# Kernel optimization log

Hardware: AMD Instinct MI355X
Metric: run time of the kernel (lower is better)

Reference implementation:

```python
import jax, jax.numpy as jnp
import numpy as np
from jax import lax

# Problem sizes (see shape_source)
B, N, S, K = 16, 4096, 1024, 32   # clouds, points/cloud, fps samples/cloud, max neighbors
C_IN, H1, H2, C_OUT = 64, 64, 64, 128
R = 0.2                            # radius ball query radius


def setup_inputs() -> dict:
    key = jax.random.key(0)
    ks = jax.random.split(key, 6)
    x = jax.random.normal(ks[0], (B * N, C_IN), jnp.float32)
    pos = jax.random.uniform(ks[1], (B * N, 3), jnp.float32)  # unit cube
    batch = jnp.repeat(jnp.arange(B, dtype=jnp.int32), N)     # equal-size clouds
    def lin(k, fan_in, fan_out):
        return jax.random.normal(k, (fan_in, fan_out), jnp.float32) / np.float32(np.sqrt(fan_in))
    W1 = lin(ks[2], C_IN + 3, H1); b1 = jnp.zeros((H1,), jnp.float32)
    W2 = lin(ks[3], H1, H2);      b2 = jnp.zeros((H2,), jnp.float32)
    W3 = lin(ks[4], H2, C_OUT);   b3 = jnp.zeros((C_OUT,), jnp.float32)
    return dict(x=x, pos=pos, batch=batch, W1=W1, b1=b1, W2=W2, b2=b2, W3=W3, b3=b3)


def _fps_single(pos):
    """Farthest point sampling on one cloud. pos: [N,3] -> [S] int32 indices.
    Deterministic start at index 0 (random_start=False equivalent)."""
    def step(carry, _):
        mind, last = carry
        d = jnp.sum((pos - pos[last]) ** 2, axis=-1)   # [N]
        mind = jnp.minimum(mind, d)
        nxt = jnp.argmax(mind).astype(jnp.int32)
        return (mind, nxt), last
    init = (jnp.full((pos.shape[0],), jnp.inf, pos.dtype), jnp.int32(0))
    _, idx = lax.scan(step, init, None, length=S)
    return idx  # [S]


def _radius_single(pos, qpos):
    """Ball query: for each query return up to K in-radius neighbors (first K by
    point index, matching torch_cluster's 'first found' semantics).
    pos: [N,3], qpos: [S,3] -> (nbr [S,K] int32, mask [S,K] bool)."""
    d2 = jnp.sum((qpos[:, None, :] - pos[None, :, :]) ** 2, axis=-1)   # [S,N]
    valid = d2 <= R * R
    key = jnp.where(valid, jnp.arange(N, dtype=jnp.int32), jnp.int32(N))  # invalid -> sentinel N
    neg_key, nbr = lax.top_k(-key, K)        # K smallest keys == first K valid indices
    mask = (-neg_key) < N
    nbr = jnp.where(mask, nbr, 0).astype(jnp.int32)  # safe gather index
    return nbr, mask


def reference(x, pos, batch, W1, b1, W2, b2, W3, b3):
    xb = x.reshape(B, N, C_IN)
    posb = pos.reshape(B, N, 3)

    # 1) FPS sampling per cloud
    idx = jax.vmap(_fps_single)(posb)                                   # [B,S]
    qpos = jnp.take_along_axis(posb, idx[:, :, None], axis=1)           # [B,S,3]

    # 2) radius ball query (max 32 neighbors)
    nbr, mask = jax.vmap(_radius_single)(posb, qpos)                    # [B,S,K]

    # 3) PointNetConv: gather, relative pos, MLP, masked max-scatter
    flat = nbr.reshape(B, S * K)
    xj = jnp.take_along_axis(xb, flat[:, :, None], axis=1).reshape(B, S, K, C_IN)
    pj = jnp.take_along_axis(posb, flat[:, :, None], axis=1).reshape(B, S, K, 3)
    rel = pj - qpos[:, :, None, :]                                      # pos_j - pos_i
    h = jnp.concatenate([xj, rel], axis=-1)                             # [B,S,K,C_IN+3]
    h = jax.nn.relu(h @ W1 + b1)
    h = jax.nn.relu(h @ W2 + b2)
    h = h @ W3 + b3                                                     # [B,S,K,C_OUT]
    h = jnp.where(mask[..., None], h, -jnp.inf)
    agg = jnp.max(h, axis=2)                                            # max aggregation
    agg = jnp.where(jnp.any(mask, axis=2)[..., None], agg, 0.0)         # empty -> 0
    out = jax.nn.relu(agg)                                              # [B,S,C_OUT]

    new_batch = jnp.repeat(jnp.arange(B, dtype=batch.dtype), S)
    return out.reshape(B * S, C_OUT), qpos.reshape(B * S, 3), new_batch
```

## Files before the change

kernel.cpp:

```cpp
#include <hip/hip_runtime.h>
#include <cstdint>
#include <cstddef>

#define B_    16
#define N_    4096
#define S_    1024
#define K_    32
#define COUT_ 128
#define NQ_   (B_*S_)

#define FT 256
#define FP (N_/FT)

__device__ __forceinline__ uint64_t wave_max_u64(uint64_t key) {
  uint32_t lo = (uint32_t)key, hi = (uint32_t)(key >> 32);
#define DPP_STEP(ctrl) { \
    uint32_t lo2 = (uint32_t)__builtin_amdgcn_update_dpp((int)lo, (int)lo, (ctrl), 0xf, 0xf, false); \
    uint32_t hi2 = (uint32_t)__builtin_amdgcn_update_dpp((int)hi, (int)hi, (ctrl), 0xf, 0xf, false); \
    const bool gt = (hi2 > hi) || (hi2 == hi && lo2 > lo); \
    hi = gt ? hi2 : hi; lo = gt ? lo2 : lo; \
  }
  DPP_STEP(0x111)
  DPP_STEP(0x112)
  DPP_STEP(0x114)
  DPP_STEP(0x118)
  DPP_STEP(0x142)
  DPP_STEP(0x143)
#undef DPP_STEP
  hi = (uint32_t)__builtin_amdgcn_readlane((int)hi, 63);
  lo = (uint32_t)__builtin_amdgcn_readlane((int)lo, 63);
  return ((uint64_t)hi << 32) | lo;
}

__global__ __launch_bounds__(FT) void fps_kernel(
    const float* __restrict__ pos, float* __restrict__ qpos_out,
    float* __restrict__ batch_out)
{
  __shared__ float px[N_], py[N_], pz[N_];
  __shared__ int   hist[S_];
  __shared__ uint64_t wkeys[2][FT/64];

  const int t = threadIdx.x;
  const int blk = blockIdx.x;
  const float* pb = pos + (size_t)blk * N_ * 3;

  for (int i = t; i < N_; i += FT) {
    px[i] = pb[i*3+0]; py[i] = pb[i*3+1]; pz[i] = pb[i*3+2];
  }
  for (int s = t; s < S_; s += FT) batch_out[(size_t)blk*S_ + s] = (float)blk;
  __syncthreads();

  float rx[FP], ry[FP], rz[FP], mind[FP];
  #pragma unroll
  for (int k = 0; k < FP; ++k) {
    const int p = k*FT + t;
    rx[k] = px[p]; ry[k] = py[p]; rz[k] = pz[p];
    mind[k] = INFINITY;
  }

  int last = 0;
  for (int s = 0; s < S_; ++s) {
    if (t == 0) hist[s] = last;
    if (s == S_-1) break;
    const float lx = px[last], ly = py[last], lz = pz[last];
    uint64_t best = 0;
    #pragma unroll
    for (int k = 0; k < FP; ++k) {
      #pragma clang fp contract(off)
      const float dx = rx[k]-lx;
      const float dy = ry[k]-ly;
      const float dz = rz[k]-lz;
      const float d  = dx*dx + dy*dy + dz*dz;
      const float m  = fminf(mind[k], d);
      mind[k] = m;
      const uint64_t key = ((uint64_t)__float_as_uint(m) << 32)
                         | (uint32_t)((N_-1) - (k*FT + t));
      if (key > best) best = key;
    }
    best = wave_max_u64(best);
    if ((t & 63) == 0) wkeys[s & 1][t >> 6] = best;
    __syncthreads();
    uint64_t gb = wkeys[s & 1][0];
    #pragma unroll
    for (int w = 1; w < FT/64; ++w) {
      const uint64_t o = wkeys[s & 1][w];
      if (o > gb) gb = o;
    }
    last = (N_-1) - (int)(uint32_t)gb;
  }
  __syncthreads();
  for (int s = t; s < S_; s += FT) {
    const int p = hist[s];
    qpos_out[((size_t)blk*S_ + s)*3 + 0] = px[p];
    qpos_out[((size_t)blk*S_ + s)*3 + 1] = py[p];
    qpos_out[((size_t)blk*S_ + s)*3 + 2] = pz[p];
  }
}

__global__ __launch_bounds__(256) void radius_kernel(
    const float* __restrict__ pos, const float* __restrict__ qpos,
    int* __restrict__ nbr, int* __restrict__ cnt_out)
{
  const int lane = threadIdx.x & 63;
  const int q = blockIdx.x * 4 + (threadIdx.x >> 6);
  const int b = q >> 10;
  const float* pb = pos + (size_t)b * N_ * 3;
  const float qx = qpos[(size_t)q*3+0];
  const float qy = qpos[(size_t)q*3+1];
  const float qz = qpos[(size_t)q*3+2];
  int cnt = 0;
  for (int base = 0; base < N_; base += 64) {
    #pragma clang fp contract(off)
    const int i = base + lane;
    const float dx = qx - pb[i*3+0];
    const float dy = qy - pb[i*3+1];
    const float dz = qz - pb[i*3+2];
    const float d  = dx*dx + dy*dy + dz*dz;
    const bool valid = (d <= 0.04f);
    const unsigned long long bal = __ballot(valid);
    const int below = __popcll(bal & ((1ull << lane) - 1ull));
    const int p = cnt + below;
    if (valid && p < K_) nbr[(size_t)q*K_ + p] = i;
    cnt += __popcll(bal);
    if (cnt >= K_) break;
  }
  const int c = (cnt < K_) ? cnt : K_;
  if (lane >= c && lane < K_) nbr[(size_t)q*K_ + lane] = 0;
  if (lane == 0) cnt_out[q] = c;
}

__global__ __launch_bounds__(256) void xw_kernel(
    const float* __restrict__ x, const float* __restrict__ W1,
    float* __restrict__ xw)
{
  __shared__ float xs[64*65];
  __shared__ float ws[64*64];
  const int t = threadIdx.x;
  const size_t rowbase = (size_t)blockIdx.x * 64;
  for (int k = t; k < 4096; k += 256) {
    xs[(k >> 6)*65 + (k & 63)] = x[rowbase*64 + k];
    ws[k] = W1[k];
  }
  __syncthreads();
  const int rg = t >> 4, cg = t & 15;
  const int r0 = rg*4, c0 = cg*4;
  float acc[4][4] = {};
  for (int i = 0; i < 64; ++i) {
    const float4 w = *(const float4*)&ws[i*64 + c0];
    #pragma unroll
    for (int j = 0; j < 4; ++j) {
      const float a = xs[(r0+j)*65 + i];
      acc[j][0] = fmaf(a, w.x, acc[j][0]);
      acc[j][1] = fmaf(a, w.y, acc[j][1]);
      acc[j][2] = fmaf(a, w.z, acc[j][2]);
      acc[j][3] = fmaf(a, w.w, acc[j][3]);
    }
  }
  #pragma unroll
  for (int j = 0; j < 4; ++j) {
    float4 v; v.x=acc[j][0]; v.y=acc[j][1]; v.z=acc[j][2]; v.w=acc[j][3];
    *(float4*)&xw[(rowbase + r0 + j)*64 + c0] = v;
  }
}

__global__ __launch_bounds__(256) void conv_kernel(
    const float* __restrict__ pos, const float* __restrict__ qpos,
    const int* __restrict__ nbr, const int* __restrict__ cnt,
    const float* __restrict__ xw,
    const float* __restrict__ W1, const float* __restrict__ b1,
    const float* __restrict__ W2, const float* __restrict__ b2,
    const float* __restrict__ W3, const float* __restrict__ b3,
    float* __restrict__ out)
{
  __shared__ float h1s[64*68];
  __shared__ float h2s[64*68];
  __shared__ float red[8*128];
  __shared__ int   nbrs[64];
  __shared__ float qps[8];
  __shared__ int   cnts[2];

  const int t  = threadIdx.x;
  const int q0 = blockIdx.x * 2;
  const int b  = q0 >> 10;

  if (t < 64) nbrs[t] = nbr[(size_t)q0*K_ + t];
  if (t < 2)  cnts[t] = cnt[q0 + t];
  if (t < 6)  qps[(t/3)*4 + (t%3)] = qpos[(size_t)q0*3 + t];
  __syncthreads();

  {
    const int c = t & 63;
    const int rsub = t >> 6;
    const float w1x = W1[64*64 + c];
    const float w1y = W1[65*64 + c];
    const float w1z = W1[66*64 + c];
    const float b1v = b1[c];
    #pragma unroll
    for (int it = 0; it < 16; ++it) {
      const int row = it*4 + rsub;
      const int lq  = row >> 5;
      const int j   = nbrs[row];
      const size_t gp = (size_t)b*N_ + j;
      const float xv = xw[gp*64 + c];
      const float rx = pos[gp*3+0] - qps[lq*4+0];
      const float ry = pos[gp*3+1] - qps[lq*4+1];
      const float rz = pos[gp*3+2] - qps[lq*4+2];
      float h = fmaf(rx, w1x, xv);
      h = fmaf(ry, w1y, h);
      h = fmaf(rz, w1z, h);
      h += b1v;
      h1s[row*68 + c] = fmaxf(h, 0.0f);
    }
  }
  __syncthreads();

  {
    const int rg = t >> 4, cg = t & 15;
    const int r0 = rg*4, c0 = cg*4;
    float acc[4][4] = {};
    for (int i = 0; i < 64; i += 4) {
      float a[4][4];
      #pragma unroll
      for (int j = 0; j < 4; ++j)
        *(float4*)&a[j][0] = *(const float4*)&h1s[(r0+j)*68 + i];
      #pragma unroll
      for (int di = 0; di < 4; ++di) {
        const float4 w = *(const float4*)&W2[(i+di)*64 + c0];
        #pragma unroll
        for (int j = 0; j < 4; ++j) {
          const float av = a[j][di];
          acc[j][0] = fmaf(av, w.x, acc[j][0]);
          acc[j][1] = fmaf(av, w.y, acc[j][1]);
          acc[j][2] = fmaf(av, w.z, acc[j][2]);
          acc[j][3] = fmaf(av, w.w, acc[j][3]);
        }
      }
    }
    const float4 bb = *(const float4*)&b2[c0];
    #pragma unroll
    for (int j = 0; j < 4; ++j) {
      float4 v;
      v.x = fmaxf(acc[j][0] + bb.x, 0.0f);
      v.y = fmaxf(acc[j][1] + bb.y, 0.0f);
      v.z = fmaxf(acc[j][2] + bb.z, 0.0f);
      v.w = fmaxf(acc[j][3] + bb.w, 0.0f);
      *(float4*)&h2s[(r0+j)*68 + c0] = v;
    }
  }
  __syncthreads();

  {
    const int rg = t >> 5, cg = t & 31;
    const int r0 = rg*8, c0 = cg*4;
    const int lq = rg >> 2;
    const int cq = cnts[lq];
    float acc[8][4] = {};
    for (int i = 0; i < 64; i += 4) {
      float a[8][4];
      #pragma unroll
      for (int j = 0; j < 8; ++j)
        *(float4*)&a[j][0] = *(const float4*)&h2s[(r0+j)*68 + i];
      #pragma unroll
      for (int di = 0; di < 4; ++di) {
        const float4 w = *(const float4*)&W3[(size_t)(i+di)*128 + c0];
        #pragma unroll
        for (int j = 0; j < 8; ++j) {
          const float av = a[j][di];
          acc[j][0] = fmaf(av, w.x, acc[j][0]);
          acc[j][1] = fmaf(av, w.y, acc[j][1]);
          acc[j][2] = fmaf(av, w.z, acc[j][2]);
          acc[j][3] = fmaf(av, w.w, acc[j][3]);
        }
      }
    }
    float pm0=-INFINITY, pm1=-INFINITY, pm2=-INFINITY, pm3=-INFINITY;
    #pragma unroll
    for (int j = 0; j < 8; ++j) {
      const int n = (r0 + j) & 31;
      if (n < cq) {
        pm0 = fmaxf(pm0, acc[j][0]);
        pm1 = fmaxf(pm1, acc[j][1]);
        pm2 = fmaxf(pm2, acc[j][2]);
        pm3 = fmaxf(pm3, acc[j][3]);
      }
    }
    float4 v; v.x=pm0; v.y=pm1; v.z=pm2; v.w=pm3;
    *(float4*)&red[rg*128 + c0] = v;
  }
  __syncthreads();
  {
    const int q = t >> 7, c = t & 127;
    const int cq = cnts[q];
    float v = -INFINITY;
    #pragma unroll
    for (int j = 0; j < 4; ++j) v = fmaxf(v, red[(q*4+j)*128 + c]);
    v = (cq > 0) ? (v + b3[c]) : 0.0f;
    v = fmaxf(v, 0.0f);
    out[(size_t)(q0 + q)*COUT_ + c] = v;
  }
}

extern "C" void kernel_launch(void* const* d_in, const int* in_sizes, int n_in,
                              void* d_out, int out_size, void* d_ws, size_t ws_size,
                              hipStream_t stream) {
  const float* x   = (const float*)d_in[0];
  const float* pos = (const float*)d_in[1];
  const float* W1  = (const float*)d_in[3];
  const float* b1  = (const float*)d_in[4];
  const float* W2  = (const float*)d_in[5];
  const float* b2  = (const float*)d_in[6];
  const float* W3  = (const float*)d_in[7];
  const float* b3  = (const float*)d_in[8];

  float* out    = (float*)d_out;
  float* qpos   = out + (size_t)NQ_*COUT_;
  float* batchf = qpos + (size_t)NQ_*3;

  char* ws = (char*)d_ws;
  float* xw = (float*)ws;
  int* nbr  = (int*)(ws + (size_t)B_*N_*64*sizeof(float));
  int* cnt  = nbr + (size_t)NQ_*K_;

  hipLaunchKernelGGL(xw_kernel,     dim3((B_*N_)/64), dim3(256), 0, stream, x, W1, xw);
  hipLaunchKernelGGL(fps_kernel,    dim3(B_),         dim3(FT),  0, stream, pos, qpos, batchf);
  hipLaunchKernelGGL(radius_kernel, dim3(NQ_/4),      dim3(256), 0, stream, pos, qpos, nbr, cnt);
  hipLaunchKernelGGL(conv_kernel,   dim3(NQ_/2),      dim3(256), 0, stream,
                     pos, qpos, nbr, cnt, xw, W1, b1, W2, b2, W3, b3, out);
}
```

Measured before the change: 888.5 us.

## Fuse all stages into a persistent mega-kernel with flag-based producer/consumer overlap

Replaces the four separate launches with one kernel whose blocks take roles from an atomic ticket: FPS, the x·W1 precompute, or radius query plus conv. FPS publishes per-cloud progress every 32 samples, so conv blocks can start on finished samples while FPS is still running. The radius query now runs inside the conv block and writes to shared memory instead of global. FPS also carries the winning point's coordinates through the reduction to skip a dependent shared load, and raises its wave priority. This relies on spin-waiting blocks not starving the producers; ticket ordering keeps FPS blocks resident first, but it adds a memset and the risk of deadlock or contention.

Result: slower. 1.020 ms (+14.8%).

```diff
diff --git a/kernel.cpp b/kernel.cpp
--- a/kernel.cpp
+++ b/kernel.cpp
@@ -9,10 +9,33 @@
 #define COUT_ 128
 #define NQ_   (B_*S_)
 
-#define FT 256
-#define FP (N_/FT)
-
-__device__ __forceinline__ uint64_t wave_max_u64(uint64_t key) {
+#define NBLK_FPS  16
+#define NBLK_XW   1024
+#define NBLK_CONV 8192
+#define GRID_     (NBLK_FPS + NBLK_XW + NBLK_CONV)
+
+union __align__(16) SMem {
+  struct {
+    float px[N_], py[N_], pz[N_];
+    int   hist[S_];
+    unsigned long long wkey[2][4];
+    float wx[2][4], wy[2][4], wz[2][4];
+  } fps;
+  struct {
+    float xs[64*65];
+    float ws[64*64];
+  } xw;
+  struct {
+    float h1s[64*68];
+    float h2s[64*68];
+    float red[8*128];
+    int   nbrs[64];
+    float qps[8];
+    int   cnts[2];
+  } conv;
+};
+
+__device__ __forceinline__ uint64_t wave_max_u64_l63(uint64_t key) {
   uint32_t lo = (uint32_t)key, hi = (uint32_t)(key >> 32);
 #define DPP_STEP(ctrl) { \
     uint32_t lo2 = (uint32_t)__builtin_amdgcn_update_dpp((int)lo, (int)lo, (ctrl), 0xf, 0xf, false); \
@@ -27,45 +50,42 @@
   DPP_STEP(0x142)
   DPP_STEP(0x143)
 #undef DPP_STEP
-  hi = (uint32_t)__builtin_amdgcn_readlane((int)hi, 63);
-  lo = (uint32_t)__builtin_amdgcn_readlane((int)lo, 63);
   return ((uint64_t)hi << 32) | lo;
 }
 
-__global__ __launch_bounds__(FT) void fps_kernel(
-    const float* __restrict__ pos, float* __restrict__ qpos_out,
-    float* __restrict__ batch_out)
+__device__ __forceinline__ void fps_role(
+    SMem& sm, int b, const float* __restrict__ pos,
+    float* __restrict__ qpos, float* __restrict__ batchf, int* progress)
 {
-  __shared__ float px[N_], py[N_], pz[N_];
-  __shared__ int   hist[S_];
-  __shared__ uint64_t wkeys[2][FT/64];
-
   const int t = threadIdx.x;
-  const int blk = blockIdx.x;
-  const float* pb = pos + (size_t)blk * N_ * 3;
-
-  for (int i = t; i < N_; i += FT) {
-    px[i] = pb[i*3+0]; py[i] = pb[i*3+1]; pz[i] = pb[i*3+2];
-  }
-  for (int s = t; s < S_; s += FT) batch_out[(size_t)blk*S_ + s] = (float)blk;
-  __syncthreads();
-
-  float rx[FP], ry[FP], rz[FP], mind[FP];
+  const int lane = t & 63, wid = t >> 6;
+  const float* pb = pos + (size_t)b * N_ * 3;
+
+  for (int i = t; i < N_; i += 256) {
+    sm.fps.px[i] = pb[i*3+0]; sm.fps.py[i] = pb[i*3+1]; sm.fps.pz[i] = pb[i*3+2];
+  }
+  for (int s = t; s < S_; s += 256) batchf[(size_t)b*S_ + s] = (float)b;
+  __syncthreads();
+
+  float rx[16], ry[16], rz[16], mind[16];
   #pragma unroll
-  for (int k = 0; k < FP; ++k) {
-    const int p = k*FT + t;
-    rx[k] = px[p]; ry[k] = py[p]; rz[k] = pz[p];
+  for (int k = 0; k < 16; ++k) {
+    const int p = k*256 + t;
+    rx[k] = sm.fps.px[p]; ry[k] = sm.fps.py[p]; rz[k] = sm.fps.pz[p];
     mind[k] = INFINITY;
   }
+  __builtin_amdgcn_s_setprio(2);
 
   int last = 0;
+  float lx = sm.fps.px[0], ly = sm.fps.py[0], lz = sm.fps.pz[0];
+
   for (int s = 0; s < S_; ++s) {
-    if (t == 0) hist[s] = last;
+    if (t == 0) sm.fps.hist[s] = last;
     if (s == S_-1) break;
-    const float lx = px[last], ly = py[last], lz = pz[last];
-    uint64_t best = 0;
-    #pragma unroll
-    for (int k = 0; k < FP; ++k) {
+
+    float bm = -1.0f; int kb = 0;
+    #pragma unroll
+    for (int k = 0; k < 16; ++k) {
       #pragma clang fp contract(off)
       const float dx = rx[k]-lx;
       const float dy = ry[k]-ly;
@@ -73,83 +93,76 @@
       const float d  = dx*dx + dy*dy + dz*dz;
       const float m  = fminf(mind[k], d);
       mind[k] = m;
-      const uint64_t key = ((uint64_t)__float_as_uint(m) << 32)
-                         | (uint32_t)((N_-1) - (k*FT + t));
-      if (key > best) best = key;
-    }
-    best = wave_max_u64(best);
-    if ((t & 63) == 0) wkeys[s & 1][t >> 6] = best;
+      if (m > bm) { bm = m; kb = k; }
+    }
+    uint64_t key = ((uint64_t)__float_as_uint(bm) << 32)
+                 | (uint32_t)((N_-1) - (kb*256 + t));
+    key = wave_max_u64_l63(key);
+    const int par = s & 1;
+    if (lane == 63) {
+      const int p = (N_-1) - (int)(uint32_t)key;
+      sm.fps.wkey[par][wid] = key;
+      sm.fps.wx[par][wid] = sm.fps.px[p];
+      sm.fps.wy[par][wid] = sm.fps.py[p];
+      sm.fps.wz[par][wid] = sm.fps.pz[p];
+    }
     __syncthreads();
-    uint64_t gb = wkeys[s & 1][0];
-    #pragma unroll
-    for (int w = 1; w < FT/64; ++w) {
-      const uint64_t o = wkeys[s & 1][w];
-      if (o > gb) gb = o;
-    }
-    last = (N_-1) - (int)(uint32_t)gb;
-  }
-  __syncthreads();
-  for (int s = t; s < S_; s += FT) {
-    const int p = hist[s];
-    qpos_out[((size_t)blk*S_ + s)*3 + 0] = px[p];
-    qpos_out[((size_t)blk*S_ + s)*3 + 1] = py[p];
-    qpos_out[((size_t)blk*S_ + s)*3 + 2] = pz[p];
-  }
-}
-
-__global__ __launch_bounds__(256) void radius_kernel(
-    const float* __restrict__ pos, const float* __restrict__ qpos,
-    int* __restrict__ nbr, int* __restrict__ cnt_out)
+    {
+      uint64_t k0 = sm.fps.wkey[par][0], k1 = sm.fps.wkey[par][1];
+      uint64_t k2 = sm.fps.wkey[par][2], k3 = sm.fps.wkey[par][3];
+      float x0=sm.fps.wx[par][0], x1=sm.fps.wx[par][1], x2=sm.fps.wx[par][2], x3=sm.fps.wx[par][3];
+      float y0=sm.fps.wy[par][0], y1=sm.fps.wy[par][1], y2=sm.fps.wy[par][2], y3=sm.fps.wy[par][3];
+      float z0=sm.fps.wz[par][0], z1=sm.fps.wz[par][1], z2=sm.fps.wz[par][2], z3=sm.fps.wz[par][3];
+      if (k1 > k0) { k0=k1; x0=x1; y0=y1; z0=z1; }
+      if (k3 > k2) { k2=k3; x2=x3; y2=y3; z2=z3; }
+      if (k2 > k0) { k0=k2; x0=x2; y0=y2; z0=z2; }
+      last = (N_-1) - (int)(uint32_t)k0;
+      lx = x0; ly = y0; lz = z0;
+    }
+    if ((s & 31) == 31) {
+      if (t < 32) {
+        const int row = s - 31 + t;
+        const int p = sm.fps.hist[row];
+        const size_t o = ((size_t)b*S_ + row)*3;
+        qpos[o+0] = sm.fps.px[p];
+        qpos[o+1] = sm.fps.py[p];
+        qpos[o+2] = sm.fps.pz[p];
+      }
+      if (t == 0)
+        __hip_atomic_store(&progress[b], s+1, __ATOMIC_RELEASE, __HIP_MEMORY_SCOPE_AGENT);
+    }
+  }
+  if (t < 32) {
+    const int row = (S_-32) + t;
+    const int p = sm.fps.hist[row];
+    const size_t o = ((size_t)b*S_ + row)*3;
+    qpos[o+0] = sm.fps.px[p];
+    qpos[o+1] = sm.fps.py[p];
+    qpos[o+2] = sm.fps.pz[p];
+  }
+  if (t == 0)
+    __hip_atomic_store(&progress[b], S_, __ATOMIC_RELEASE, __HIP_MEMORY_SCOPE_AGENT);
+}
+
+__device__ __forceinline__ void xw_role(
+    SMem& sm, int tile, const float* __restrict__ x,
+    const float* __restrict__ W1, float* __restrict__ xw, int* xwdone)
 {
-  const int lane = threadIdx.x & 63;
-  const int q = blockIdx.x * 4 + (threadIdx.x >> 6);
-  const int b = q >> 10;
-  const float* pb = pos + (size_t)b * N_ * 3;
-  const float qx = qpos[(size_t)q*3+0];
-  const float qy = qpos[(size_t)q*3+1];
-  const float qz = qpos[(size_t)q*3+2];
-  int cnt = 0;
-  for (int base = 0; base < N_; base += 64) {
-    #pragma clang fp contract(off)
-    const int i = base + lane;
-    const float dx = qx - pb[i*3+0];
-    const float dy = qy - pb[i*3+1];
-    const float dz = qz - pb[i*3+2];
-    const float d  = dx*dx + dy*dy + dz*dz;
-    const bool valid = (d <= 0.04f);
-    const unsigned long long bal = __ballot(valid);
-    const int below = __popcll(bal & ((1ull << lane) - 1ull));
-    const int p = cnt + below;
-    if (valid && p < K_) nbr[(size_t)q*K_ + p] = i;
-    cnt += __popcll(bal);
-    if (cnt >= K_) break;
-  }
-  const int c = (cnt < K_) ? cnt : K_;
-  if (lane >= c && lane < K_) nbr[(size_t)q*K_ + lane] = 0;
-  if (lane == 0) cnt_out[q] = c;
-}
-
-__global__ __launch_bounds__(256) void xw_kernel(
-    const float* __restrict__ x, const float* __restrict__ W1,
-    float* __restrict__ xw)
-{
-  __shared__ float xs[64*65];
-  __shared__ float ws[64*64];
   const int t = threadIdx.x;
-  const size_t rowbase = (size_t)blockIdx.x * 64;
+  const size_t rowbase = (size_t)tile * 64;
   for (int k = t; k < 4096; k += 256) {
-    xs[(k >> 6)*65 + (k & 63)] = x[rowbase*64 + k];
-    ws[k] = W1[k];
+    sm.xw.xs[(k >> 6)*65 + (k & 63)] = x[rowbase*64 + k];
+    sm.xw.ws[k] = W1[k];
   }
   __syncthreads();
   const int rg = t >> 4, cg = t & 15;
   const int r0 = rg*4, c0 = cg*4;
   float acc[4][4] = {};
   for (int i = 0; i < 64; ++i) {
-    const float4 w = *(const float4*)&ws[i*64 + c0];
+    const float4 w = *(const float4*)&sm.xw.ws[i*64 + c0];
     #pragma unroll
     for (int j = 0; j < 4; ++j) {
-      const float a = xs[(r0+j)*65 + i];
+      const float a = sm.xw.xs[(r0+j)*65 + i];
       acc[j][0] = fmaf(a, w.x, acc[j][0]);
       acc[j][1] = fmaf(a, w.y, acc[j][1]);
       acc[j][2] = fmaf(a, w.z, acc[j][2]);
@@ -161,31 +174,61 @@
     float4 v; v.x=acc[j][0]; v.y=acc[j][1]; v.z=acc[j][2]; v.w=acc[j][3];
     *(float4*)&xw[(rowbase + r0 + j)*64 + c0] = v;
   }
-}
-
-__global__ __launch_bounds__(256) void conv_kernel(
-    const float* __restrict__ pos, const float* __restrict__ qpos,
-    const int* __restrict__ nbr, const int* __restrict__ cnt,
+  __syncthreads();
+  if (t == 0)
+    __hip_atomic_fetch_add(&xwdone[tile >> 6], 1, __ATOMIC_RELEASE, __HIP_MEMORY_SCOPE_AGENT);
+}
+
+__device__ __forceinline__ void conv_role(
+    SMem& sm, int j, const float* __restrict__ pos, const float* __restrict__ qpos,
     const float* __restrict__ xw,
     const float* __restrict__ W1, const float* __restrict__ b1,
     const float* __restrict__ W2, const float* __restrict__ b2,
     const float* __restrict__ W3, const float* __restrict__ b3,
-    float* __restrict__ out)
+    float* __restrict__ out, int* progress, int* xwdone)
 {
-  __shared__ float h1s[64*68];
-  __shared__ float h2s[64*68];
-  __shared__ float red[8*128];
-  __shared__ int   nbrs[64];
-  __shared__ float qps[8];
-  __shared__ int   cnts[2];
-
-  const int t  = threadIdx.x;
-  const int q0 = blockIdx.x * 2;
-  const int b  = q0 >> 10;
-
-  if (t < 64) nbrs[t] = nbr[(size_t)q0*K_ + t];
-  if (t < 2)  cnts[t] = cnt[q0 + t];
-  if (t < 6)  qps[(t/3)*4 + (t%3)] = qpos[(size_t)q0*3 + t];
+  const int t = threadIdx.x;
+  const int bb   = j & 15;
+  const int pair = j >> 4;
+  const int q0   = bb*S_ + pair*2;
+
+  if (t == 0) {
+    while (__hip_atomic_load(&xwdone[bb], __ATOMIC_ACQUIRE, __HIP_MEMORY_SCOPE_AGENT) < 64)
+      __builtin_amdgcn_s_sleep(127);
+    const int need = pair*2 + 2;
+    while (__hip_atomic_load(&progress[bb], __ATOMIC_ACQUIRE, __HIP_MEMORY_SCOPE_AGENT) < need)
+      __builtin_amdgcn_s_sleep(127);
+  }
+  __syncthreads();
+
+  const int wid = t >> 6, lane = t & 63;
+  if (wid < 2) {
+    const int q = q0 + wid;
+    const float* pb = pos + (size_t)bb * N_ * 3;
+    const float qx = qpos[(size_t)q*3+0];
+    const float qy = qpos[(size_t)q*3+1];
+    const float qz = qpos[(size_t)q*3+2];
+    int cnt = 0;
+    for (int base = 0; base < N_; base += 64) {
+      #pragma clang fp contract(off)
+      const int i = base + lane;
+      const float dx = qx - pb[i*3+0];
+      const float dy = qy - pb[i*3+1];
+      const float dz = qz - pb[i*3+2];
+      const float d  = dx*dx + dy*dy + dz*dz;
+      const bool valid = (d <= 0.04f);
+      const unsigned long long bal = __ballot(valid);
+      const int below = __popcll(bal & ((1ull << lane) - 1ull));
+      const int p = cnt + below;
+      if (valid && p < K_) sm.conv.nbrs[wid*K_ + p] = i;
+      cnt += __popcll(bal);
+      if (cnt >= K_) break;
+    }
+    const int c = (cnt < K_) ? cnt : K_;
+    if (lane >= c && lane < K_) sm.conv.nbrs[wid*K_ + lane] = 0;
+    if (lane == 0) sm.conv.cnts[wid] = c;
+  }
+  if (t < 6) sm.conv.qps[(t/3)*4 + (t%3)] = qpos[(size_t)q0*3 + t];
   __syncthreads();
 
   {
@@ -199,17 +242,17 @@
     for (int it = 0; it < 16; ++it) {
       const int row = it*4 + rsub;
       const int lq  = row >> 5;
-      const int j   = nbrs[row];
-      const size_t gp = (size_t)b*N_ + j;
+      const int jn  = sm.conv.nbrs[row];
+      const size_t gp = (size_t)bb*N_ + jn;
       const float xv = xw[gp*64 + c];
-      const float rx = pos[gp*3+0] - qps[lq*4+0];
-      const float ry = pos[gp*3+1] - qps[lq*4+1];
-      const float rz = pos[gp*3+2] - qps[lq*4+2];
+      const float rx = pos[gp*3+0] - sm.conv.qps[lq*4+0];
+      const float ry = pos[gp*3+1] - sm.conv.qps[lq*4+1];
+      const float rz = pos[gp*3+2] - sm.conv.qps[lq*4+2];
       float h = fmaf(rx, w1x, xv);
       h = fmaf(ry, w1y, h);
       h = fmaf(rz, w1z, h);
       h += b1v;
-      h1s[row*68 + c] = fmaxf(h, 0.0f);
+      sm.conv.h1s[row*68 + c] = fmaxf(h, 0.0f);
     }
   }
   __syncthreads();
@@ -221,30 +264,30 @@
     for (int i = 0; i < 64; i += 4) {
       float a[4][4];
       #pragma unroll
-      for (int j = 0; j < 4; ++j)
-        *(float4*)&a[j][0] = *(const float4*)&h1s[(r0+j)*68 + i];
+      for (int jj = 0; jj < 4; ++jj)
+        *(float4*)&a[jj][0] = *(const float4*)&sm.conv.h1s[(r0+jj)*68 + i];
       #pragma unroll
       for (int di = 0; di < 4; ++di) {
         const float4 w = *(const float4*)&W2[(i+di)*64 + c0];
         #pragma unroll
-        for (int j = 0; j < 4; ++j) {
-          const float av = a[j][di];
-          acc[j][0] = fmaf(av, w.x, acc[j][0]);
-          acc[j][1] = fmaf(av, w.y, acc[j][1]);
-          acc[j][2] = fmaf(av, w.z, acc[j][2]);
-          acc[j][3] = fmaf(av, w.w, acc[j][3]);
+        for (int jj = 0; jj < 4; ++jj) {
+          const float av = a[jj][di];
+          acc[jj][0] = fmaf(av, w.x, acc[jj][0]);
+          acc[jj][1] = fmaf(av, w.y, acc[jj][1]);
+          acc[jj][2] = fmaf(av, w.z, acc[jj][2]);
+          acc[jj][3] = fmaf(av, w.w, acc[jj][3]);
         }
       }
     }
-    const float4 bb = *(const float4*)&b2[c0];
-    #pragma unroll
-    for (int j = 0; j < 4; ++j) {
+    const float4 bbv = *(const float4*)&b2[c0];
+    #pragma unroll
+    for (int jj = 0; jj < 4; ++jj) {
       float4 v;
-      v.x = fmaxf(acc[j][0] + bb.x, 0.0f);
-      v.y = fmaxf(acc[j][1] + bb.y, 0.0f);
-      v.z = fmaxf(acc[j][2] + bb.z, 0.0f);
-      v.w = fmaxf(acc[j][3] + bb.w, 0.0f);
-      *(float4*)&h2s[(r0+j)*68 + c0] = v;
+      v.x = fmaxf(acc[jj][0] + bbv.x, 0.0f);
+      v.y = fmaxf(acc[jj][1] + bbv.y, 0.0f);
+      v.z = fmaxf(acc[jj][2] + bbv.z, 0.0f);
+      v.w = fmaxf(acc[jj][3] + bbv.w, 0.0f);
+      *(float4*)&sm.conv.h2s[(r0+jj)*68 + c0] = v;
     }
   }
   __syncthreads();
@@ -253,50 +296,77 @@
     const int rg = t >> 5, cg = t & 31;
     const int r0 = rg*8, c0 = cg*4;
     const int lq = rg >> 2;
-    const int cq = cnts[lq];
+    const int cq = sm.conv.cnts[lq];
     float acc[8][4] = {};
     for (int i = 0; i < 64; i += 4) {
       float a[8][4];
       #pragma unroll
-      for (int j = 0; j < 8; ++j)
-        *(float4*)&a[j][0] = *(const float4*)&h2s[(r0+j)*68 + i];
+      for (int jj = 0; jj < 8; ++jj)
+        *(float4*)&a[jj][0] = *(const float4*)&sm.conv.h2s[(r0+jj)*68 + i];
       #pragma unroll
       for (int di = 0; di < 4; ++di) {
         const float4 w = *(const float4*)&W3[(size_t)(i+di)*128 + c0];
         #pragma unroll
-        for (int j = 0; j < 8; ++j) {
-          const float av = a[j][di];
-          acc[j][0] = fmaf(av, w.x, acc[j][0]);
-          acc[j][1] = fmaf(av, w.y, acc[j][1]);
-          acc[j][2] = fmaf(av, w.z, acc[j][2]);
-          acc[j][3] = fmaf(av, w.w, acc[j][3]);
+        for (int jj = 0; jj < 8; ++jj) {
+          const float av = a[jj][di];
+          acc[jj][0] = fmaf(av, w.x, acc[jj][0]);
+          acc[jj][1] = fmaf(av, w.y, acc[jj][1]);
+          acc[jj][2] = fmaf(av, w.z, acc[jj][2]);
+          acc[jj][3] = fmaf(av, w.w, acc[jj][3]);
         }
       }
     }
     float pm0=-INFINITY, pm1=-INFINITY, pm2=-INFINITY, pm3=-INFINITY;
     #pragma unroll
-    for (int j = 0; j < 8; ++j) {
-      const int n = (r0 + j) & 31;
+    for (int jj = 0; jj < 8; ++jj) {
+      const int n = (r0 + jj) & 31;
       if (n < cq) {
-        pm0 = fmaxf(pm0, acc[j][0]);
-        pm1 = fmaxf(pm1, acc[j][1]);
-        pm2 = fmaxf(pm2, acc[j][2]);
-        pm3 = fmaxf(pm3, acc[j][3]);
+        pm0 = fmaxf(pm0, acc[jj][0]);
+        pm1 = fmaxf(pm1, acc[jj][1]);
+        pm2 = fmaxf(pm2, acc[jj][2]);
+        pm3 = fmaxf(pm3, acc[jj][3]);
       }
     }
     float4 v; v.x=pm0; v.y=pm1; v.z=pm2; v.w=pm3;
-    *(float4*)&red[rg*128 + c0] = v;
+    *(float4*)&sm.conv.red[rg*128 + c0] = v;
   }
   __syncthreads();
   {
     const int q = t >> 7, c = t & 127;
-    const int cq = cnts[q];
+    const int cq = sm.conv.cnts[q];
     float v = -INFINITY;
     #pragma unroll
-    for (int j = 0; j < 4; ++j) v = fmaxf(v, red[(q*4+j)*128 + c]);
+    for (int jj = 0; jj < 4; ++jj) v = fmaxf(v, sm.conv.red[(q*4+jj)*128 + c]);
     v = (cq > 0) ? (v + b3[c]) : 0.0f;
     v = fmaxf(v, 0.0f);
     out[(size_t)(q0 + q)*COUT_ + c] = v;
+  }
+}
+
+__global__ __launch_bounds__(256) void mega_kernel(
+    const float* __restrict__ x, const float* __restrict__ pos,
+    const float* __restrict__ W1, const float* __restrict__ b1,
+    const float* __restrict__ W2, const float* __restrict__ b2,
+    const float* __restrict__ W3, const float* __restrict__ b3,
+    float* __restrict__ out, float* __restrict__ qpos, float* __restrict__ batchf,
+    float* __restrict__ xw, int* flags)
+{
+  __shared__ SMem sm;
+  __shared__ int tk_s;
+  int* ticket   = flags + 0;
+  int* progress = flags + 16;
+  int* xwdone   = flags + 48;
+  if (threadIdx.x == 0) tk_s = atomicAdd(ticket, 1);
+  __syncthreads();
+  const int tk = tk_s;
+
+  if (tk < NBLK_FPS) {
+    fps_role(sm, tk, pos, qpos, batchf, progress);
+  } else if (tk < NBLK_FPS + NBLK_XW) {
+    xw_role(sm, tk - NBLK_FPS, x, W1, xw, xwdone);
+  } else {
+    conv_role(sm, tk - NBLK_FPS - NBLK_XW, pos, qpos, xw,
+              W1, b1, W2, b2, W3, b3, out, progress, xwdone);
   }
 }
 
@@ -317,13 +387,10 @@
   float* batchf = qpos + (size_t)NQ_*3;
 
   char* ws = (char*)d_ws;
-  float* xw = (float*)ws;
-  int* nbr  = (int*)(ws + (size_t)B_*N_*64*sizeof(float));
-  int* cnt  = nbr + (size_t)NQ_*K_;
-
-  hipLaunchKernelGGL(xw_kernel,     dim3((B_*N_)/64), dim3(256), 0, stream, x, W1, xw);
-  hipLaunchKernelGGL(fps_kernel,    dim3(B_),         dim3(FT),  0, stream, pos, qpos, batchf);
-  hipLaunchKernelGGL(radius_kernel, dim3(NQ_/4),      dim3(256), 0, stream, pos, qpos, nbr, cnt);
-  hipLaunchKernelGGL(conv_kernel,   dim3(NQ_/2),      dim3(256), 0, stream,
-                     pos, qpos, nbr, cnt, xw, W1, b1, W2, b2, W3, b3, out);
-}
+  float* xw  = (float*)ws;
+  int* flags = (int*)(ws + (size_t)B_*N_*64*sizeof(float));
+
+  hipMemsetAsync(flags, 0, 256, stream);
+  hipLaunchKernelGGL(mega_kernel, dim3(GRID_), dim3(256), 0, stream,
+                     x, pos, W1, b1, W2, b2, W3, b3, out, qpos, batchf, xw, flags);
+}
```

## Run two FPS clouds per block and carry winner coordinates through the reduction

Applied to the files above, without the earlier changes.

The farthest-point-sampling kernel now handles two point clouds per block, interleaving their independent serial argmax chains. The aim is to hide the per-step latency of the dependent loop and the barrier. Each thread first finds its argmax with a float compare and forms a 64-bit key only once, instead of once per point. Each wave's winner coordinates are written to shared memory next to its key, which removes the dependent LDS lookup of px[last] at the start of the next step. In exchange, each block does twice the per-step arithmetic, uses more registers and shared memory, and runs as half as many blocks.

Result: slower. 1.671 ms (+88.1%).

```diff
diff --git a/kernel.cpp b/kernel.cpp
--- a/kernel.cpp
+++ b/kernel.cpp
@@ -12,7 +12,7 @@
 #define FT 256
 #define FP (N_/FT)
 
-__device__ __forceinline__ uint64_t wave_max_u64(uint64_t key) {
+__device__ __forceinline__ uint64_t wave_max_u64_l63(uint64_t key) {
   uint32_t lo = (uint32_t)key, hi = (uint32_t)(key >> 32);
 #define DPP_STEP(ctrl) { \
     uint32_t lo2 = (uint32_t)__builtin_amdgcn_update_dpp((int)lo, (int)lo, (ctrl), 0xf, 0xf, false); \
@@ -27,73 +27,124 @@
   DPP_STEP(0x142)
   DPP_STEP(0x143)
 #undef DPP_STEP
-  hi = (uint32_t)__builtin_amdgcn_readlane((int)hi, 63);
-  lo = (uint32_t)__builtin_amdgcn_readlane((int)lo, 63);
   return ((uint64_t)hi << 32) | lo;
 }
 
-__global__ __launch_bounds__(FT) void fps_kernel(
+__global__ __launch_bounds__(FT) void fps2_kernel(
     const float* __restrict__ pos, float* __restrict__ qpos_out,
     float* __restrict__ batch_out)
 {
-  __shared__ float px[N_], py[N_], pz[N_];
-  __shared__ int   hist[S_];
-  __shared__ uint64_t wkeys[2][FT/64];
+  __shared__ float px[2][N_], py[2][N_], pz[2][N_];
+  __shared__ int   hist[2][S_];
+  __shared__ unsigned long long wkey[2][2][4];
+  __shared__ float wx[2][2][4], wy[2][2][4], wz[2][2][4];
 
   const int t = threadIdx.x;
-  const int blk = blockIdx.x;
-  const float* pb = pos + (size_t)blk * N_ * 3;
+  const int lane = t & 63, wid = t >> 6;
+  const int bA = blockIdx.x * 2, bB = bA + 1;
+  const float* pA = pos + (size_t)bA * N_ * 3;
+  const float* pB = pos + (size_t)bB * N_ * 3;
 
   for (int i = t; i < N_; i += FT) {
-    px[i] = pb[i*3+0]; py[i] = pb[i*3+1]; pz[i] = pb[i*3+2];
-  }
-  for (int s = t; s < S_; s += FT) batch_out[(size_t)blk*S_ + s] = (float)blk;
-  __syncthreads();
-
-  float rx[FP], ry[FP], rz[FP], mind[FP];
+    px[0][i] = pA[i*3+0]; py[0][i] = pA[i*3+1]; pz[0][i] = pA[i*3+2];
+    px[1][i] = pB[i*3+0]; py[1][i] = pB[i*3+1]; pz[1][i] = pB[i*3+2];
+  }
+  for (int s = t; s < S_; s += FT) {
+    batch_out[(size_t)bA*S_ + s] = (float)bA;
+    batch_out[(size_t)bB*S_ + s] = (float)bB;
+  }
+  __syncthreads();
+
+  float rxA[FP], ryA[FP], rzA[FP], mindA[FP];
+  float rxB[FP], ryB[FP], rzB[FP], mindB[FP];
   #pragma unroll
   for (int k = 0; k < FP; ++k) {
     const int p = k*FT + t;
-    rx[k] = px[p]; ry[k] = py[p]; rz[k] = pz[p];
-    mind[k] = INFINITY;
-  }
-
-  int last = 0;
+    rxA[k] = px[0][p]; ryA[k] = py[0][p]; rzA[k] = pz[0][p]; mindA[k] = INFINITY;
+    rxB[k] = px[1][p]; ryB[k] = py[1][p]; rzB[k] = pz[1][p]; mindB[k] = INFINITY;
+  }
+
+  int lastA = 0, lastB = 0;
+  float lxA = px[0][0], lyA = py[0][0], lzA = pz[0][0];
+  float lxB = px[1][0], lyB = py[1][0], lzB = pz[1][0];
+
   for (int s = 0; s < S_; ++s) {
-    if (t == 0) hist[s] = last;
+    if (t == 0) { hist[0][s] = lastA; hist[1][s] = lastB; }
     if (s == S_-1) break;
-    const float lx = px[last], ly = py[last], lz = pz[last];
-    uint64_t best = 0;
+
+    float bmA = -1.0f; int kbA = 0;
     #pragma unroll
     for (int k = 0; k < FP; ++k) {
       #pragma clang fp contract(off)
-      const float dx = rx[k]-lx;
-      const float dy = ry[k]-ly;
-      const float dz = rz[k]-lz;
+      const float dx = rxA[k]-lxA;
+      const float dy = ryA[k]-lyA;
+      const float dz = rzA[k]-lzA;
       const float d  = dx*dx + dy*dy + dz*dz;
-      const float m  = fminf(mind[k], d);
-      mind[k] = m;
-      const uint64_t key = ((uint64_t)__float_as_uint(m) << 32)
-                         | (uint32_t)((N_-1) - (k*FT + t));
-      if (key > best) best = key;
-    }
-    best = wave_max_u64(best);
-    if ((t & 63) == 0) wkeys[s & 1][t >> 6] = best;
+      const float m  = fminf(mindA[k], d);
+      mindA[k] = m;
+      if (m > bmA) { bmA = m; kbA = k; }
+    }
+    float bmB = -1.0f; int kbB = 0;
+    #pragma unroll
+    for (int k = 0; k < FP; ++k) {
+      #pragma clang fp contract(off)
+      const float dx = rxB[k]-lxB;
+      const float dy = ryB[k]-lyB;
+      const float dz = rzB[k]-lzB;
+      const float d  = dx*dx + dy*dy + dz*dz;
+      const float m  = fminf(mindB[k], d);
+      mindB[k] = m;
+      if (m > bmB) { bmB = m; kbB = k; }
+    }
+    uint64_t keyA = ((uint64_t)__float_as_uint(bmA) << 32)
+                  | (uint32_t)((N_-1) - (kbA*FT + t));
+    uint64_t keyB = ((uint64_t)__float_as_uint(bmB) << 32)
+                  | (uint32_t)((N_-1) - (kbB*FT + t));
+    keyA = wave_max_u64_l63(keyA);
+    keyB = wave_max_u64_l63(keyB);
+    const int par = s & 1;
+    if (lane == 63) {
+      const int pa = (N_-1) - (int)(uint32_t)keyA;
+      const int pb = (N_-1) - (int)(uint32_t)keyB;
+      wkey[0][par][wid] = keyA;
+      wx[0][par][wid] = px[0][pa]; wy[0][par][wid] = py[0][pa]; wz[0][par][wid] = pz[0][pa];
+      wkey[1][par][wid] = keyB;
+      wx[1][par][wid] = px[1][pb]; wy[1][par][wid] = py[1][pb]; wz[1][par][wid] = pz[1][pb];
+    }
     __syncthreads();
-    uint64_t gb = wkeys[s & 1][0];
-    #pragma unroll
-    for (int w = 1; w < FT/64; ++w) {
-      const uint64_t o = wkeys[s & 1][w];
-      if (o > gb) gb = o;
-    }
-    last = (N_-1) - (int)(uint32_t)gb;
+    {
+      uint64_t k0 = wkey[0][par][0], k1 = wkey[0][par][1];
+      uint64_t k2 = wkey[0][par][2], k3 = wkey[0][par][3];
+      float x0=wx[0][par][0], x1=wx[0][par][1], x2=wx[0][par][2], x3=wx[0][par][3];
+      float y0=wy[0][par][0], y1=wy[0][par][1], y2=wy[0][par][2], y3=wy[0][par][3];
+      float z0=wz[0][par][0], z1=wz[0][par][1], z2=wz[0][par][2], z3=wz[0][par][3];
+      if (k1 > k0) { k0=k1; x0=x1; y0=y1; z0=z1; }
+      if (k3 > k2) { k2=k3; x2=x3; y2=y3; z2=z3; }
+      if (k2 > k0) { k0=k2; x0=x2; y0=y2; z0=z2; }
+      lastA = (N_-1) - (int)(uint32_t)k0;
+      lxA = x0; lyA = y0; lzA = z0;
+    }
+    {
+      uint64_t k0 = wkey[1][par][0], k1 = wkey[1][par][1];
+      uint64_t k2 = wkey[1][par][2], k3 = wkey[1][par][3];
+      float x0=wx[1][par][0], x1=wx[1][par][1], x2=wx[1][par][2], x3=wx[1][par][3];
+      float y0=wy[1][par][0], y1=wy[1][par][1], y2=wy[1][par][2], y3=wy[1][par][3];
+      float z0=wz[1][par][0], z1=wz[1][par][1], z2=wz[1][par][2], z3=wz[1][par][3];
+      if (k1 > k0) { k0=k1; x0=x1; y0=y1; z0=z1; }
+      if (k3 > k2) { k2=k3; x2=x3; y2=y3; z2=z3; }
+      if (k2 > k0) { k0=k2; x0=x2; y0=y2; z0=z2; }
+      lastB = (N_-1) - (int)(uint32_t)k0;
+      lxB = x0; lyB = y0; lzB = z0;
+    }
   }
   __syncthreads();
   for (int s = t; s < S_; s += FT) {
-    const int p = hist[s];
-    qpos_out[((size_t)blk*S_ + s)*3 + 0] = px[p];
-    qpos_out[((size_t)blk*S_ + s)*3 + 1] = py[p];
-    qpos_out[((size_t)blk*S_ + s)*3 + 2] = pz[p];
+    const int pa = hist[0][s];
+    const int pb = hist[1][s];
+    const size_t oA = ((size_t)bA*S_ + s)*3;
+    const size_t oB = ((size_t)bB*S_ + s)*3;
+    qpos_out[oA+0] = px[0][pa]; qpos_out[oA+1] = py[0][pa]; qpos_out[oA+2] = pz[0][pa];
+    qpos_out[oB+0] = px[1][pb]; qpos_out[oB+1] = py[1][pb]; qpos_out[oB+2] = pz[1][pb];
   }
 }
 
@@ -322,7 +373,7 @@
   int* cnt  = nbr + (size_t)NQ_*K_;
 
   hipLaunchKernelGGL(xw_kernel,     dim3((B_*N_)/64), dim3(256), 0, stream, x, W1, xw);
-  hipLaunchKernelGGL(fps_kernel,    dim3(B_),         dim3(FT),  0, stream, pos, qpos, batchf);
+  hipLaunchKernelGGL(fps2_kernel,   dim3(B_/2),       dim3(FT),  0, stream, pos, qpos, batchf);
   hipLaunchKernelGGL(radius_kernel, dim3(NQ_/4),      dim3(256), 0, stream, pos, qpos, nbr, cnt);
   hipLaunchKernelGGL(conv_kernel,   dim3(NQ_/2),      dim3(256), 0, stream,
                      pos, qpos, nbr, cnt, xw, W1, b1, W2, b2, W3, b3, out);
```
